# Kernel tuning notes

Hardware: AMD Instinct MI355X
Metric: run time of the kernel (lower is better)

Reference implementation:

```python
import jax, jax.numpy as jnp
import numpy as np

B, M, C = 8, 1024, 768


def setup_inputs() -> dict:
    key = jax.random.key(0)
    ks = jax.random.split(key, 10)
    s = 0.02
    return {
        "layout_x": jax.random.normal(ks[0], (B, M, C), jnp.float32),
        "text_x": jax.random.normal(ks[1], (B, M, C), jnp.float32),
        "mask": jax.random.randint(ks[2], (B, M), 0, 2).astype(jnp.float32),
        "Wqkv": jax.random.normal(ks[3], (C, 3 * C), jnp.float32) * s,
        "bqkv": jnp.zeros((3 * C,), jnp.float32),
        "Wq": jax.random.normal(ks[4], (C, C), jnp.float32) * s,
        "bq": jnp.zeros((C,), jnp.float32),
        "Wkv": jax.random.normal(ks[5], (C, 2 * C), jnp.float32) * s,
        "bkv": jnp.zeros((2 * C,), jnp.float32),
        "Wffn": jax.random.normal(ks[6], (C, C), jnp.float32) * s,
        "bffn": jnp.zeros((C,), jnp.float32),
    }


def _masked_attn(q, k, v, pair_mask, scale):
    # pair_mask: [B,M,M] True where valid (mask_i * mask_j != 0)
    scores = jnp.einsum("bmd,bnd->bmn", q, k) * scale  # [B,M,M]
    scores = jnp.where(pair_mask, scores, jnp.float32(-10000.0))
    attn = jax.nn.softmax(scores, axis=-1)
    return jnp.einsum("bmn,bnd->bmd", attn, v)


def reference(layout_x, text_x, mask, Wqkv, bqkv, Wq, bq, Wkv, bkv, Wffn, bffn):
    dim = layout_x.shape[-1]
    scale = dim ** (-0.5)
    # mask repeated over C then mask@mask.T / C  ==  outer product of 1D masks
    pair = (mask[:, :, None] * mask[:, None, :]) != 0  # [B,M,M] bool, True=keep

    # self-attention on layout_x
    qkv = layout_x @ Wqkv + bqkv  # [B,M,3C]
    q, k, v = jnp.split(qkv, 3, axis=-1)
    layout_o = _masked_attn(q, k, v, pair, scale)

    # cross-attention: q from layout output, k/v from text_x
    cq = layout_o @ Wq + bq
    kv = text_x @ Wkv + bkv  # [B,M,2C]
    ck, cv = jnp.split(kv, 2, axis=-1)
    merge = _masked_attn(cq, ck, cv, pair, scale)

    return merge @ Wffn + bffn
```

## Files before the change

### kernel.cpp

```cpp
#include <hip/hip_runtime.h>
#include <math.h>

#define BDIM 8
#define MDIM 1024
#define CDIM 768
#define ROWS (BDIM * MDIM)

typedef __attribute__((ext_vector_type(8))) short short8;
typedef __attribute__((ext_vector_type(8))) unsigned short ushort8;
typedef __attribute__((ext_vector_type(4))) float f32x4;

#define MFMA16(a, b, c) __builtin_amdgcn_mfma_f32_16x16x32_bf16((a), (b), (c), 0, 0, 0)

__device__ __forceinline__ unsigned short f2bf(float f) {
  unsigned u = __float_as_uint(f);
  return (unsigned short)((u + 0x7FFFu + ((u >> 16) & 1u)) >> 16);
}

__global__ __launch_bounds__(256) void convert2_bf16(
    const float* __restrict__ s0, const float* __restrict__ s1,
    unsigned short* __restrict__ d0, unsigned short* __restrict__ d1, int n) {
  const float* src = blockIdx.y ? s1 : s0;
  unsigned short* dst = blockIdx.y ? d1 : d0;
  const int i = (blockIdx.x * 256 + threadIdx.x) * 8;
  if (i >= n) return;
  const float4 a = *(const float4*)(src + i);
  const float4 b = *(const float4*)(src + i + 4);
  ushort8 o;
  o[0] = f2bf(a.x); o[1] = f2bf(a.y); o[2] = f2bf(a.z); o[3] = f2bf(a.w);
  o[4] = f2bf(b.x); o[5] = f2bf(b.y); o[6] = f2bf(b.z); o[7] = f2bf(b.w);
  *(ushort8*)(dst + i) = o;
}

__global__ __launch_bounds__(256) void transpose_w_all(
    const float* __restrict__ W0, const float* __restrict__ W1,
    const float* __restrict__ W2, const float* __restrict__ W3,
    unsigned short* __restrict__ D0, unsigned short* __restrict__ D1,
    unsigned short* __restrict__ D2, unsigned short* __restrict__ D3) {
  int x = blockIdx.x;
  const float* W; unsigned short* D; int N;
  if (x < 72)       { W = W0; D = D0; N = 2304; }
  else if (x < 96)  { W = W1; D = D1; N = 768;  x -= 72; }
  else if (x < 144) { W = W2; D = D2; N = 1536; x -= 96; }
  else              { W = W3; D = D3; N = 768;  x -= 144; }
  __shared__ unsigned short t[32][33];
  const int tx = threadIdx.x, ty = threadIdx.y;
  const int n0 = x * 32, k0 = blockIdx.y * 32;
#pragma unroll
  for (int i = 0; i < 4; ++i)
    t[ty + i * 8][tx] = f2bf(W[(size_t)(k0 + ty + i * 8) * N + n0 + tx]);
  __syncthreads();
#pragma unroll
  for (int i = 0; i < 4; ++i)
    D[(size_t)(n0 + ty + i * 8) * CDIM + k0 + tx] = t[tx][ty + i * 8];
}

__device__ __forceinline__ void stage64(
    const unsigned short* __restrict__ g, int ld, int k0,
    unsigned short* lds, int wave, int lane) {
  const int gchunk = (lane & 7) ^ (lane >> 3);
#pragma unroll
  for (int j = 0; j < 4; ++j) {
    const int grp = wave * 4 + j;
    const unsigned short* gp =
        g + (size_t)(grp * 8 + (lane >> 3)) * ld + k0 + gchunk * 8;
    __builtin_amdgcn_global_load_lds(
        (const __attribute__((address_space(1))) unsigned int*)gp,
        (__attribute__((address_space(3))) unsigned int*)(lds + grp * 512),
        16, 0, 0);
  }
}

__device__ __forceinline__ void mfma_loop64(
    const unsigned short* __restrict__ A, int lda,
    const unsigned short* __restrict__ Bt, int ldb, int K,
    unsigned short* As, unsigned short* Bs, f32x4 acc[4][4],
    int wave, int lane) {
  const int wx = wave & 1, wy = wave >> 1;
  const int quad = lane >> 4, l16 = lane & 15;
  for (int k0 = 0; k0 < K; k0 += 64) {
    stage64(A, lda, k0, As, wave, lane);
    stage64(Bt, ldb, k0, Bs, wave, lane);
    __syncthreads();
#pragma unroll
    for (int h = 0; h < 2; ++h) {
      const int slot = ((((h << 2) | quad) ^ (l16 & 7))) * 8;
      short8 afr[4], bfr[4];
#pragma unroll
      for (int mt = 0; mt < 4; ++mt)
        afr[mt] = *(const short8*)&As[(wy * 64 + mt * 16 + l16) * 64 + slot];
#pragma unroll
      for (int nt = 0; nt < 4; ++nt)
        bfr[nt] = *(const short8*)&Bs[(wx * 64 + nt * 16 + l16) * 64 + slot];
#pragma unroll
      for (int mt = 0; mt < 4; ++mt)
#pragma unroll
        for (int nt = 0; nt < 4; ++nt)
          acc[mt][nt] = MFMA16(afr[mt], bfr[nt], acc[mt][nt]);
    }
    __syncthreads();
  }
}

template <bool BF16OUT, bool TRANS_LAST>
__global__ __launch_bounds__(256, 3) void gemm_mfma(
    const unsigned short* __restrict__ A, const unsigned short* __restrict__ Bt,
    const float* __restrict__ bias, void* __restrict__ Yv,
    unsigned short* __restrict__ vTdst) {
  __shared__ __align__(16) unsigned short As[128 * 64];
  __shared__ __align__(16) unsigned short Bs[128 * 64];
  const int c0 = blockIdx.x * 128;
  const int m0 = blockIdx.y * 128;
  const int tid = threadIdx.x;
  const int wave = tid >> 6, lane = tid & 63;
  const int wx = wave & 1, wy = wave >> 1;
  const int quad = lane >> 4, l16 = lane & 15;

  const f32x4 vzero = {0.f, 0.f, 0.f, 0.f};
  f32x4 acc[4][4];
#pragma unroll
  for (int mt = 0; mt < 4; ++mt)
#pragma unroll
    for (int nt = 0; nt < 4; ++nt) acc[mt][nt] = vzero;

  mfma_loop64(A + (size_t)m0 * CDIM, CDIM, Bt + (size_t)c0 * CDIM, CDIM, CDIM,
              As, Bs, acc, wave, lane);

  const int slice = c0 / 768;
  if (TRANS_LAST && slice == (int)(gridDim.x / 6) - 1) {
#pragma unroll
    for (int mt = 0; mt < 4; ++mt) {
      const int row0 = m0 + wy * 64 + mt * 16 + quad * 4;
      const int b = row0 >> 10, n0 = row0 & 1023;
#pragma unroll
      for (int nt = 0; nt < 4; ++nt) {
        const int gcol = c0 + wx * 64 + nt * 16 + l16;
        const int d = gcol - slice * 768;
        const float bv = bias[gcol];
        uint2 o;
        o.x = (unsigned)f2bf(acc[mt][nt][0] + bv) |
              ((unsigned)f2bf(acc[mt][nt][1] + bv) << 16);
        o.y = (unsigned)f2bf(acc[mt][nt][2] + bv) |
              ((unsigned)f2bf(acc[mt][nt][3] + bv) << 16);
        *(uint2*)&vTdst[((size_t)b * CDIM + d) * MDIM + n0] = o;
      }
    }
  } else {
    const size_t sbase = (size_t)slice * ROWS * 768;
#pragma unroll
    for (int mt = 0; mt < 4; ++mt)
#pragma unroll
      for (int nt = 0; nt < 4; ++nt) {
        const int gcol = c0 + wx * 64 + nt * 16 + l16;
        const int lcol = gcol - slice * 768;
        const float bv = bias[gcol];
#pragma unroll
        for (int rg = 0; rg < 4; ++rg) {
          const int row = m0 + wy * 64 + mt * 16 + quad * 4 + rg;
          const float v = acc[mt][nt][rg] + bv;
          if (BF16OUT)
            ((unsigned short*)Yv)[sbase + (size_t)row * 768 + lcol] = f2bf(v);
          else
            ((float*)Yv)[sbase + (size_t)row * 768 + lcol] = v;
        }
      }
  }
}

__global__ __launch_bounds__(256, 3) void gemm_qk(
    const unsigned short* __restrict__ Qb, const unsigned short* __restrict__ Kb,
    const float* __restrict__ mask, unsigned short* __restrict__ S, float scale) {
  __shared__ __align__(16) unsigned short As[128 * 64];
  __shared__ __align__(16) unsigned short Bs[128 * 64];
  const int c0 = blockIdx.x * 128;
  const int m0 = blockIdx.y * 128;
  const int b = blockIdx.z;
  const int tid = threadIdx.x;
  const int wave = tid >> 6, lane = tid & 63;
  const int wx = wave & 1, wy = wave >> 1;
  const int quad = lane >> 4, l16 = lane & 15;

  const f32x4 vzero = {0.f, 0.f, 0.f, 0.f};
  f32x4 acc[4][4];
#pragma unroll
  for (int mt = 0; mt < 4; ++mt)
#pragma unroll
    for (int nt = 0; nt < 4; ++nt) acc[mt][nt] = vzero;

  mfma_loop64(Qb + ((size_t)b * MDIM + m0) * CDIM, CDIM,
              Kb + ((size_t)b * MDIM + c0) * CDIM, CDIM, CDIM,
              As, Bs, acc, wave, lane);

  const float* maskb = mask + b * MDIM;
  float mrow[4][4];
#pragma unroll
  for (int mt = 0; mt < 4; ++mt)
#pragma unroll
    for (int rg = 0; rg < 4; ++rg)
      mrow[mt][rg] = maskb[m0 + wy * 64 + mt * 16 + quad * 4 + rg];
  unsigned short* Sb = S + (size_t)b * MDIM * MDIM;
#pragma unroll
  for (int nt = 0; nt < 4; ++nt) {
    const int col = c0 + wx * 64 + nt * 16 + l16;
    const float mcol = maskb[col];
#pragma unroll
    for (int mt = 0; mt < 4; ++mt)
#pragma unroll
      for (int rg = 0; rg < 4; ++rg) {
        const int row = m0 + wy * 64 + mt * 16 + quad * 4 + rg;
        const float sv =
            (mrow[mt][rg] * mcol != 0.f) ? acc[mt][nt][rg] * scale : -10000.0f;
        Sb[(size_t)row * MDIM + col] = f2bf(sv);
      }
  }
}

__global__ __launch_bounds__(256) void softmax_row(unsigned short* __restrict__ S) {
  __shared__ float red[2][4];
  unsigned short* p = S + (size_t)blockIdx.x * MDIM;
  const int t = threadIdx.x;
  const int wave = t >> 6, lane = t & 63;
  const uint2 u = *(const uint2*)(p + t * 4);
  const float v0 = __uint_as_float((u.x & 0xFFFFu) << 16);
  const float v1 = __uint_as_float(u.x & 0xFFFF0000u);
  const float v2 = __uint_as_float((u.y & 0xFFFFu) << 16);
  const float v3 = __uint_as_float(u.y & 0xFFFF0000u);
  float mx = fmaxf(fmaxf(v0, v1), fmaxf(v2, v3));
  for (int off = 1; off < 64; off <<= 1) mx = fmaxf(mx, __shfl_xor(mx, off, 64));
  if (lane == 0) red[0][wave] = mx;
  __syncthreads();
  mx = fmaxf(fmaxf(red[0][0], red[0][1]), fmaxf(red[0][2], red[0][3]));
  const float e0 = __expf(v0 - mx), e1 = __expf(v1 - mx);
  const float e2 = __expf(v2 - mx), e3 = __expf(v3 - mx);
  float s = e0 + e1 + e2 + e3;
  for (int off = 1; off < 64; off <<= 1) s += __shfl_xor(s, off, 64);
  if (lane == 0) red[1][wave] = s;
  __syncthreads();
  const float inv = 1.f / (red[1][0] + red[1][1] + red[1][2] + red[1][3]);
  uint2 o;
  o.x = (unsigned)f2bf(e0 * inv) | ((unsigned)f2bf(e1 * inv) << 16);
  o.y = (unsigned)f2bf(e2 * inv) | ((unsigned)f2bf(e3 * inv) << 16);
  *(uint2*)(p + t * 4) = o;
}

__global__ __launch_bounds__(256, 3) void attn_pv(
    const unsigned short* __restrict__ P, const unsigned short* __restrict__ vT,
    unsigned short* __restrict__ O) {
  __shared__ __align__(16) unsigned short As[128 * 64];
  __shared__ __align__(16) unsigned short Bs[128 * 64];
  const int c0 = blockIdx.x * 128;
  const int m0 = blockIdx.y * 128;
  const int b = blockIdx.z;
  const int tid = threadIdx.x;
  const int wave = tid >> 6, lane = tid & 63;
  const int wx = wave & 1, wy = wave >> 1;
  const int quad = lane >> 4, l16 = lane & 15;

  const f32x4 vzero = {0.f, 0.f, 0.f, 0.f};
  f32x4 acc[4][4];
#pragma unroll
  for (int mt = 0; mt < 4; ++mt)
#pragma unroll
    for (int nt = 0; nt < 4; ++nt) acc[mt][nt] = vzero;

  mfma_loop64(P + ((size_t)b * MDIM + m0) * MDIM, MDIM,
              vT + ((size_t)b * CDIM + c0) * MDIM, MDIM, MDIM,
              As, Bs, acc, wave, lane);

#pragma unroll
  for (int mt = 0; mt < 4; ++mt)
#pragma unroll
    for (int nt = 0; nt < 4; ++nt)
#pragma unroll
      for (int rg = 0; rg < 4; ++rg) {
        const int row = m0 + wy * 64 + mt * 16 + quad * 4 + rg;
        const int col = c0 + wx * 64 + nt * 16 + l16;
        O[(size_t)(b * MDIM + row) * CDIM + col] = f2bf(acc[mt][nt][rg]);
      }
}

extern "C" void kernel_launch(void* const* d_in, const int* in_sizes, int n_in,
                              void* d_out, int out_size, void* d_ws, size_t ws_size,
                              hipStream_t stream) {
  const float* layout_x = (const float*)d_in[0];
  const float* text_x   = (const float*)d_in[1];
  const float* maskp    = (const float*)d_in[2];
  const float* Wqkv     = (const float*)d_in[3];
  const float* bqkv     = (const float*)d_in[4];
  const float* Wq       = (const float*)d_in[5];
  const float* bq       = (const float*)d_in[6];
  const float* Wkv      = (const float*)d_in[7];
  const float* bkv      = (const float*)d_in[8];
  const float* Wffn     = (const float*)d_in[9];
  const float* bffn     = (const float*)d_in[10];
  float* out = (float*)d_out;
  char* ws = (char*)d_ws;

  const float scale = 1.0f / sqrtf((float)CDIM);

  unsigned short* xlb    = (unsigned short*)(ws);
  unsigned short* xtb    = (unsigned short*)(ws + 12582912);
  unsigned short* Wqkv_t = (unsigned short*)(ws + 25165824);
  unsigned short* Wq_t   = (unsigned short*)(ws + 28704768);
  unsigned short* Wkv_t  = (unsigned short*)(ws + 29884416);
  unsigned short* Wffn_t = (unsigned short*)(ws + 32243712);
  unsigned short* Qb     = (unsigned short*)(ws + 33423360);
  unsigned short* Kb     = (unsigned short*)(ws + 46006272);
  unsigned short* Vb     = (unsigned short*)(ws + 58589184);
  unsigned short* vT     = (unsigned short*)(ws + 71172096);
  unsigned short* S      = (unsigned short*)(ws + 83755008);
  unsigned short* attn1  = xlb;
  unsigned short* cqb    = Vb;
  unsigned short* Kc     = Qb;

  convert2_bf16<<<dim3(ROWS * CDIM / 2048, 2), 256, 0, stream>>>(
      layout_x, text_x, xlb, xtb, ROWS * CDIM);
  transpose_w_all<<<dim3(168, 24), dim3(32, 8), 0, stream>>>(
      Wqkv, Wq, Wkv, Wffn, Wqkv_t, Wq_t, Wkv_t, Wffn_t);

  gemm_mfma<true, true><<<dim3(18, 64), 256, 0, stream>>>(
      xlb, Wqkv_t, bqkv, Qb, vT);
  gemm_qk<<<dim3(8, 8, BDIM), 256, 0, stream>>>(Qb, Kb, maskp, S, scale);
  softmax_row<<<ROWS, 256, 0, stream>>>(S);
  attn_pv<<<dim3(6, 8, BDIM), 256, 0, stream>>>(S, vT, attn1);
  gemm_mfma<true, false><<<dim3(6, 64), 256, 0, stream>>>(
      attn1, Wq_t, bq, cqb, vT);
  gemm_mfma<true, true><<<dim3(12, 64), 256, 0, stream>>>(
      xtb, Wkv_t, bkv, Kc, vT);
  gemm_qk<<<dim3(8, 8, BDIM), 256, 0, stream>>>(cqb, Kc, maskp, S, scale);
  softmax_row<<<ROWS, 256, 0, stream>>>(S);
  attn_pv<<<dim3(6, 8, BDIM), 256, 0, stream>>>(S, vT, attn1);
  gemm_mfma<false, false><<<dim3(6, 64), 256, 0, stream>>>(
      attn1, Wffn_t, bffn, out, vT);
}
```

Baseline: 338.4 us.

## Fuse softmax into QK and PV epilogues, merge prologue and projection launches

```diff
diff --git a/kernel.cpp b/kernel.cpp
--- a/kernel.cpp
+++ b/kernel.cpp
@@ -17,42 +17,51 @@
   return (unsigned short)((u + 0x7FFFu + ((u >> 16) & 1u)) >> 16);
 }
 
-__global__ __launch_bounds__(256) void convert2_bf16(
-    const float* __restrict__ s0, const float* __restrict__ s1,
-    unsigned short* __restrict__ d0, unsigned short* __restrict__ d1, int n) {
-  const float* src = blockIdx.y ? s1 : s0;
-  unsigned short* dst = blockIdx.y ? d1 : d0;
-  const int i = (blockIdx.x * 256 + threadIdx.x) * 8;
-  if (i >= n) return;
-  const float4 a = *(const float4*)(src + i);
-  const float4 b = *(const float4*)(src + i + 4);
-  ushort8 o;
-  o[0] = f2bf(a.x); o[1] = f2bf(a.y); o[2] = f2bf(a.z); o[3] = f2bf(a.w);
-  o[4] = f2bf(b.x); o[5] = f2bf(b.y); o[6] = f2bf(b.z); o[7] = f2bf(b.w);
-  *(ushort8*)(dst + i) = o;
-}
-
-__global__ __launch_bounds__(256) void transpose_w_all(
+__global__ __launch_bounds__(256) void prologue(
+    const float* __restrict__ xl, const float* __restrict__ xt,
+    unsigned short* __restrict__ dxl, unsigned short* __restrict__ dxt,
     const float* __restrict__ W0, const float* __restrict__ W1,
     const float* __restrict__ W2, const float* __restrict__ W3,
     unsigned short* __restrict__ D0, unsigned short* __restrict__ D1,
-    unsigned short* __restrict__ D2, unsigned short* __restrict__ D3) {
-  int x = blockIdx.x;
-  const float* W; unsigned short* D; int N;
-  if (x < 72)       { W = W0; D = D0; N = 2304; }
-  else if (x < 96)  { W = W1; D = D1; N = 768;  x -= 72; }
-  else if (x < 144) { W = W2; D = D2; N = 1536; x -= 96; }
-  else              { W = W3; D = D3; N = 768;  x -= 144; }
-  __shared__ unsigned short t[32][33];
-  const int tx = threadIdx.x, ty = threadIdx.y;
-  const int n0 = x * 32, k0 = blockIdx.y * 32;
-#pragma unroll
-  for (int i = 0; i < 4; ++i)
-    t[ty + i * 8][tx] = f2bf(W[(size_t)(k0 + ty + i * 8) * N + n0 + tx]);
-  __syncthreads();
-#pragma unroll
-  for (int i = 0; i < 4; ++i)
-    D[(size_t)(n0 + ty + i * 8) * CDIM + k0 + tx] = t[tx][ty + i * 8];
+    unsigned short* __restrict__ D2, unsigned short* __restrict__ D3,
+    float* __restrict__ rowsum) {
+  const int bx = blockIdx.x;
+  const int tid = threadIdx.x;
+  if (bx < 6144) {
+    const float* src = bx < 3072 ? xl : xt;
+    unsigned short* dst = bx < 3072 ? dxl : dxt;
+    const int i = ((bx < 3072 ? bx : bx - 3072) * 256 + tid) * 8;
+    const float4 a = *(const float4*)(src + i);
+    const float4 b = *(const float4*)(src + i + 4);
+    ushort8 o;
+    o[0] = f2bf(a.x); o[1] = f2bf(a.y); o[2] = f2bf(a.z); o[3] = f2bf(a.w);
+    o[4] = f2bf(b.x); o[5] = f2bf(b.y); o[6] = f2bf(b.z); o[7] = f2bf(b.w);
+    *(ushort8*)(dst + i) = o;
+  } else if (bx < 6152) {
+    const int i = ((bx - 6144) * 256 + tid) * 8;
+    const float4 z = {0.f, 0.f, 0.f, 0.f};
+    *(float4*)(rowsum + i) = z;
+    *(float4*)(rowsum + i + 4) = z;
+  } else {
+    int x = bx - 6152;
+    int bxx = x % 168;
+    const int k0 = (x / 168) * 32;
+    const float* W; unsigned short* D; int N;
+    if (bxx < 72)       { W = W0; D = D0; N = 2304; }
+    else if (bxx < 96)  { W = W1; D = D1; N = 768;  bxx -= 72; }
+    else if (bxx < 144) { W = W2; D = D2; N = 1536; bxx -= 96; }
+    else                { W = W3; D = D3; N = 768;  bxx -= 144; }
+    __shared__ unsigned short t[32][33];
+    const int tx = tid & 31, ty = tid >> 5;
+    const int n0 = bxx * 32;
+#pragma unroll
+    for (int i = 0; i < 4; ++i)
+      t[ty + i * 8][tx] = f2bf(W[(size_t)(k0 + ty + i * 8) * N + n0 + tx]);
+    __syncthreads();
+#pragma unroll
+    for (int i = 0; i < 4; ++i)
+      D[(size_t)(n0 + ty + i * 8) * CDIM + k0 + tx] = t[tx][ty + i * 8];
+  }
 }
 
 __device__ __forceinline__ void stage64(
@@ -102,32 +111,14 @@
   }
 }
 
-template <bool BF16OUT, bool TRANS_LAST>
-__global__ __launch_bounds__(256, 3) void gemm_mfma(
-    const unsigned short* __restrict__ A, const unsigned short* __restrict__ Bt,
-    const float* __restrict__ bias, void* __restrict__ Yv,
-    unsigned short* __restrict__ vTdst) {
-  __shared__ __align__(16) unsigned short As[128 * 64];
-  __shared__ __align__(16) unsigned short Bs[128 * 64];
-  const int c0 = blockIdx.x * 128;
-  const int m0 = blockIdx.y * 128;
-  const int tid = threadIdx.x;
-  const int wave = tid >> 6, lane = tid & 63;
+__device__ __forceinline__ void proj_epilogue(
+    f32x4 acc[4][4], const float* __restrict__ bias,
+    unsigned short* __restrict__ Y, unsigned short* __restrict__ vTd,
+    int c0, int m0, int lastSlice, int trans, int wave, int lane) {
   const int wx = wave & 1, wy = wave >> 1;
   const int quad = lane >> 4, l16 = lane & 15;
-
-  const f32x4 vzero = {0.f, 0.f, 0.f, 0.f};
-  f32x4 acc[4][4];
-#pragma unroll
-  for (int mt = 0; mt < 4; ++mt)
-#pragma unroll
-    for (int nt = 0; nt < 4; ++nt) acc[mt][nt] = vzero;
-
-  mfma_loop64(A + (size_t)m0 * CDIM, CDIM, Bt + (size_t)c0 * CDIM, CDIM, CDIM,
-              As, Bs, acc, wave, lane);
-
   const int slice = c0 / 768;
-  if (TRANS_LAST && slice == (int)(gridDim.x / 6) - 1) {
+  if (trans && slice == lastSlice) {
 #pragma unroll
     for (int mt = 0; mt < 4; ++mt) {
       const int row0 = m0 + wy * 64 + mt * 16 + quad * 4;
@@ -142,7 +133,7 @@
               ((unsigned)f2bf(acc[mt][nt][1] + bv) << 16);
         o.y = (unsigned)f2bf(acc[mt][nt][2] + bv) |
               ((unsigned)f2bf(acc[mt][nt][3] + bv) << 16);
-        *(uint2*)&vTdst[((size_t)b * CDIM + d) * MDIM + n0] = o;
+        *(uint2*)&vTd[((size_t)b * CDIM + d) * MDIM + n0] = o;
       }
     }
   } else {
@@ -157,19 +148,107 @@
 #pragma unroll
         for (int rg = 0; rg < 4; ++rg) {
           const int row = m0 + wy * 64 + mt * 16 + quad * 4 + rg;
-          const float v = acc[mt][nt][rg] + bv;
-          if (BF16OUT)
-            ((unsigned short*)Yv)[sbase + (size_t)row * 768 + lcol] = f2bf(v);
-          else
-            ((float*)Yv)[sbase + (size_t)row * 768 + lcol] = v;
+          Y[sbase + (size_t)row * 768 + lcol] = f2bf(acc[mt][nt][rg] + bv);
         }
       }
   }
 }
 
-__global__ __launch_bounds__(256, 3) void gemm_qk(
+__device__ __forceinline__ void swizzle_mc(int lin, int* m0, int* c0) {
+  const int xcd = lin & 7, j = lin >> 3;
+  *m0 = (xcd * 8 + (j & 7)) * 128;
+  *c0 = (j >> 3) * 128;
+}
+
+__global__ __launch_bounds__(256, 4) void gemm_proj(
+    const unsigned short* __restrict__ A, const unsigned short* __restrict__ Bt,
+    const float* __restrict__ bias, unsigned short* __restrict__ Y,
+    unsigned short* __restrict__ vTd, int trans) {
+  __shared__ __align__(16) unsigned short As[128 * 64];
+  __shared__ __align__(16) unsigned short Bs[128 * 64];
+  int m0, c0;
+  swizzle_mc(blockIdx.y * gridDim.x + blockIdx.x, &m0, &c0);
+  const int tid = threadIdx.x;
+  const int wave = tid >> 6, lane = tid & 63;
+  const f32x4 vzero = {0.f, 0.f, 0.f, 0.f};
+  f32x4 acc[4][4];
+#pragma unroll
+  for (int mt = 0; mt < 4; ++mt)
+#pragma unroll
+    for (int nt = 0; nt < 4; ++nt) acc[mt][nt] = vzero;
+  mfma_loop64(A + (size_t)m0 * CDIM, CDIM, Bt + (size_t)c0 * CDIM, CDIM, CDIM,
+              As, Bs, acc, wave, lane);
+  proj_epilogue(acc, bias, Y, vTd, c0, m0, (int)(gridDim.x / 6) - 1, trans,
+                wave, lane);
+}
+
+__global__ __launch_bounds__(256, 4) void gemm_proj_dual(
+    const unsigned short* __restrict__ A0, const unsigned short* __restrict__ B0,
+    const float* __restrict__ b0, unsigned short* __restrict__ Y0,
+    const unsigned short* __restrict__ A1, const unsigned short* __restrict__ B1,
+    const float* __restrict__ b1, unsigned short* __restrict__ Y1,
+    unsigned short* __restrict__ vTd) {
+  __shared__ __align__(16) unsigned short As[128 * 64];
+  __shared__ __align__(16) unsigned short Bs[128 * 64];
+  int lin = blockIdx.x;
+  const unsigned short *A, *Bt;
+  const float* bias;
+  unsigned short* Y;
+  int gx, trans;
+  if (lin < 384) { A = A0; Bt = B0; bias = b0; Y = Y0; gx = 6;  trans = 0; }
+  else { lin -= 384; A = A1; Bt = B1; bias = b1; Y = Y1; gx = 12; trans = 1; }
+  int m0, c0;
+  swizzle_mc(lin, &m0, &c0);
+  const int tid = threadIdx.x;
+  const int wave = tid >> 6, lane = tid & 63;
+  const f32x4 vzero = {0.f, 0.f, 0.f, 0.f};
+  f32x4 acc[4][4];
+#pragma unroll
+  for (int mt = 0; mt < 4; ++mt)
+#pragma unroll
+    for (int nt = 0; nt < 4; ++nt) acc[mt][nt] = vzero;
+  mfma_loop64(A + (size_t)m0 * CDIM, CDIM, Bt + (size_t)c0 * CDIM, CDIM, CDIM,
+              As, Bs, acc, wave, lane);
+  proj_epilogue(acc, bias, Y, vTd, c0, m0, gx / 6 - 1, trans, wave, lane);
+}
+
+__global__ __launch_bounds__(256, 4) void gemm_ffn(
+    const unsigned short* __restrict__ A, const unsigned short* __restrict__ Bt,
+    const float* __restrict__ bias, float* __restrict__ Y) {
+  __shared__ __align__(16) unsigned short As[128 * 64];
+  __shared__ __align__(16) unsigned short Bs[128 * 64];
+  int m0, c0;
+  swizzle_mc(blockIdx.y * gridDim.x + blockIdx.x, &m0, &c0);
+  const int tid = threadIdx.x;
+  const int wave = tid >> 6, lane = tid & 63;
+  const int wx = wave & 1, wy = wave >> 1;
+  const int quad = lane >> 4, l16 = lane & 15;
+  const f32x4 vzero = {0.f, 0.f, 0.f, 0.f};
+  f32x4 acc[4][4];
+#pragma unroll
+  for (int mt = 0; mt < 4; ++mt)
+#pragma unroll
+    for (int nt = 0; nt < 4; ++nt) acc[mt][nt] = vzero;
+  mfma_loop64(A + (size_t)m0 * CDIM, CDIM, Bt + (size_t)c0 * CDIM, CDIM, CDIM,
+              As, Bs, acc, wave, lane);
+#pragma unroll
+  for (int mt = 0; mt < 4; ++mt)
+#pragma unroll
+    for (int nt = 0; nt < 4; ++nt) {
+      const int col = c0 + wx * 64 + nt * 16 + l16;
+      const float bv = bias[col];
+#pragma unroll
+      for (int rg = 0; rg < 4; ++rg) {
+        const int row = m0 + wy * 64 + mt * 16 + quad * 4 + rg;
+        Y[(size_t)row * 768 + col] = acc[mt][nt][rg] + bv;
+      }
+    }
+}
+
+__global__ __launch_bounds__(256, 4) void gemm_qk(
     const unsigned short* __restrict__ Qb, const unsigned short* __restrict__ Kb,
-    const float* __restrict__ mask, unsigned short* __restrict__ S, float scale) {
+    const float* __restrict__ mask, unsigned short* __restrict__ S, float scale,
+    float* __restrict__ rowsum) {
   __shared__ __align__(16) unsigned short As[128 * 64];
   __shared__ __align__(16) unsigned short Bs[128 * 64];
   const int c0 = blockIdx.x * 128;
@@ -192,12 +271,14 @@
               As, Bs, acc, wave, lane);
 
   const float* maskb = mask + b * MDIM;
-  float mrow[4][4];
-#pragma unroll
-  for (int mt = 0; mt < 4; ++mt)
-#pragma unroll
-    for (int rg = 0; rg < 4; ++rg)
+  float mrow[4][4], rsum[4][4];
+#pragma unroll
+  for (int mt = 0; mt < 4; ++mt)
+#pragma unroll
+    for (int rg = 0; rg < 4; ++rg) {
       mrow[mt][rg] = maskb[m0 + wy * 64 + mt * 16 + quad * 4 + rg];
+      rsum[mt][rg] = 0.f;
+    }
   unsigned short* Sb = S + (size_t)b * MDIM * MDIM;
 #pragma unroll
   for (int nt = 0; nt < 4; ++nt) {
@@ -208,44 +289,33 @@
 #pragma unroll
       for (int rg = 0; rg < 4; ++rg) {
         const int row = m0 + wy * 64 + mt * 16 + quad * 4 + rg;
-        const float sv =
-            (mrow[mt][rg] * mcol != 0.f) ? acc[mt][nt][rg] * scale : -10000.0f;
-        Sb[(size_t)row * MDIM + col] = f2bf(sv);
+        const float e = (mrow[mt][rg] * mcol != 0.f)
+                            ? __expf(acc[mt][nt][rg] * scale)
+                            : 1e-30f;
+        Sb[(size_t)row * MDIM + col] = f2bf(e);
+        rsum[mt][rg] += e;
       }
   }
-}
-
-__global__ __launch_bounds__(256) void softmax_row(unsigned short* __restrict__ S) {
-  __shared__ float red[2][4];
-  unsigned short* p = S + (size_t)blockIdx.x * MDIM;
-  const int t = threadIdx.x;
-  const int wave = t >> 6, lane = t & 63;
-  const uint2 u = *(const uint2*)(p + t * 4);
-  const float v0 = __uint_as_float((u.x & 0xFFFFu) << 16);
-  const float v1 = __uint_as_float(u.x & 0xFFFF0000u);
-  const float v2 = __uint_as_float((u.y & 0xFFFFu) << 16);
-  const float v3 = __uint_as_float(u.y & 0xFFFF0000u);
-  float mx = fmaxf(fmaxf(v0, v1), fmaxf(v2, v3));
-  for (int off = 1; off < 64; off <<= 1) mx = fmaxf(mx, __shfl_xor(mx, off, 64));
-  if (lane == 0) red[0][wave] = mx;
-  __syncthreads();
-  mx = fmaxf(fmaxf(red[0][0], red[0][1]), fmaxf(red[0][2], red[0][3]));
-  const float e0 = __expf(v0 - mx), e1 = __expf(v1 - mx);
-  const float e2 = __expf(v2 - mx), e3 = __expf(v3 - mx);
-  float s = e0 + e1 + e2 + e3;
-  for (int off = 1; off < 64; off <<= 1) s += __shfl_xor(s, off, 64);
-  if (lane == 0) red[1][wave] = s;
-  __syncthreads();
-  const float inv = 1.f / (red[1][0] + red[1][1] + red[1][2] + red[1][3]);
-  uint2 o;
-  o.x = (unsigned)f2bf(e0 * inv) | ((unsigned)f2bf(e1 * inv) << 16);
-  o.y = (unsigned)f2bf(e2 * inv) | ((unsigned)f2bf(e3 * inv) << 16);
-  *(uint2*)(p + t * 4) = o;
-}
-
-__global__ __launch_bounds__(256, 3) void attn_pv(
+  for (int off = 1; off < 16; off <<= 1) {
+#pragma unroll
+    for (int mt = 0; mt < 4; ++mt)
+#pragma unroll
+      for (int rg = 0; rg < 4; ++rg)
+        rsum[mt][rg] += __shfl_xor(rsum[mt][rg], off, 64);
+  }
+  if (l16 == 0) {
+    float* rsb = rowsum + (b << 10) + m0 + wy * 64;
+#pragma unroll
+    for (int mt = 0; mt < 4; ++mt)
+#pragma unroll
+      for (int rg = 0; rg < 4; ++rg)
+        atomicAdd(&rsb[mt * 16 + quad * 4 + rg], rsum[mt][rg]);
+  }
+}
+
+__global__ __launch_bounds__(256, 4) void attn_pv(
     const unsigned short* __restrict__ P, const unsigned short* __restrict__ vT,
-    unsigned short* __restrict__ O) {
+    unsigned short* __restrict__ O, const float* __restrict__ rowsum) {
   __shared__ __align__(16) unsigned short As[128 * 64];
   __shared__ __align__(16) unsigned short Bs[128 * 64];
   const int c0 = blockIdx.x * 128;
@@ -267,6 +337,13 @@
               vT + ((size_t)b * CDIM + c0) * MDIM, MDIM, MDIM,
               As, Bs, acc, wave, lane);
 
+  const float* rsb = rowsum + (b << 10) + m0 + wy * 64;
+  float inv[4][4];
+#pragma unroll
+  for (int mt = 0; mt < 4; ++mt)
+#pragma unroll
+    for (int rg = 0; rg < 4; ++rg)
+      inv[mt][rg] = 1.f / rsb[mt * 16 + quad * 4 + rg];
 #pragma unroll
   for (int mt = 0; mt < 4; ++mt)
 #pragma unroll
@@ -275,7 +352,8 @@
       for (int rg = 0; rg < 4; ++rg) {
         const int row = m0 + wy * 64 + mt * 16 + quad * 4 + rg;
         const int col = c0 + wx * 64 + nt * 16 + l16;
-        O[(size_t)(b * MDIM + row) * CDIM + col] = f2bf(acc[mt][nt][rg]);
+        O[(size_t)(b * MDIM + row) * CDIM + col] =
+            f2bf(acc[mt][nt][rg] * inv[mt][rg]);
       }
 }
 
@@ -306,30 +384,23 @@
   unsigned short* Wffn_t = (unsigned short*)(ws + 32243712);
   unsigned short* Qb     = (unsigned short*)(ws + 33423360);
   unsigned short* Kb     = (unsigned short*)(ws + 46006272);
-  unsigned short* Vb     = (unsigned short*)(ws + 58589184);
+  unsigned short* cqb    = (unsigned short*)(ws + 58589184);
   unsigned short* vT     = (unsigned short*)(ws + 71172096);
   unsigned short* S      = (unsigned short*)(ws + 83755008);
   unsigned short* attn1  = xlb;
-  unsigned short* cqb    = Vb;
   unsigned short* Kc     = Qb;
-
-  convert2_bf16<<<dim3(ROWS * CDIM / 2048, 2), 256, 0, stream>>>(
-      layout_x, text_x, xlb, xtb, ROWS * CDIM);
-  transpose_w_all<<<dim3(168, 24), dim3(32, 8), 0, stream>>>(
-      Wqkv, Wq, Wkv, Wffn, Wqkv_t, Wq_t, Wkv_t, Wffn_t);
-
-  gemm_mfma<true, true><<<dim3(18, 64), 256, 0, stream>>>(
-      xlb, Wqkv_t, bqkv, Qb, vT);
-  gemm_qk<<<dim3(8, 8, BDIM), 256, 0, stream>>>(Qb, Kb, maskp, S, scale);
-  softmax_row<<<ROWS, 256, 0, stream>>>(S);
-  attn_pv<<<dim3(6, 8, BDIM), 256, 0, stream>>>(S, vT, attn1);
-  gemm_mfma<true, false><<<dim3(6, 64), 256, 0, stream>>>(
-      attn1, Wq_t, bq, cqb, vT);
-  gemm_mfma<true, true><<<dim3(12, 64), 256, 0, stream>>>(
-      xtb, Wkv_t, bkv, Kc, vT);
-  gemm_qk<<<dim3(8, 8, BDIM), 256, 0, stream>>>(cqb, Kc, maskp, S, scale);
-  softmax_row<<<ROWS, 256, 0, stream>>>(S);
-  attn_pv<<<dim3(6, 8, BDIM), 256, 0, stream>>>(S, vT, attn1);
-  gemm_mfma<false, false><<<dim3(6, 64), 256, 0, stream>>>(
-      attn1, Wffn_t, bffn, out, vT);
-}
+  float* rowsum1 = out;
+  float* rowsum2 = out + 8192;
+
+  prologue<<<10184, 256, 0, stream>>>(layout_x, text_x, xlb, xtb,
+                                      Wqkv, Wq, Wkv, Wffn,
+                                      Wqkv_t, Wq_t, Wkv_t, Wffn_t, rowsum1);
+  gemm_proj<<<dim3(18, 64), 256, 0, stream>>>(xlb, Wqkv_t, bqkv, Qb, vT, 1);
+  gemm_qk<<<dim3(8, 8, BDIM), 256, 0, stream>>>(Qb, Kb, maskp, S, scale, rowsum1);
+  attn_pv<<<dim3(6, 8, BDIM), 256, 0, stream>>>(S, vT, attn1, rowsum1);
+  gemm_proj_dual<<<1152, 256, 0, stream>>>(attn1, Wq_t, bq, cqb,
+                                           xtb, Wkv_t, bkv, Kc, vT);
+  gemm_qk<<<dim3(8, 8, BDIM), 256, 0, stream>>>(cqb, Kc, maskp, S, scale, rowsum2);
+  attn_pv<<<dim3(6, 8, BDIM), 256, 0, stream>>>(S, vT, attn1, rowsum2);
+  gemm_ffn<<<dim3(6, 64), 256, 0, stream>>>(attn1, Wffn_t, bffn, out);
+}
```

Measured after the change: 311.5 us. -8.0%, faster.
